# Optimization experiments

Measured on AMD Instinct MI355X. Metric: run time of the kernel, lower is better.

The kernel has to match this reference:

```python
import jax, jax.numpy as jnp
import numpy as np

D = 768      # embedding_dim
H = 12       # num_heads
HS = D // H  # head_size = 64
B, T, TC = 8, 1024, 256
FF = 4 * D
EPS = 1e-5


def _layernorm(x, w, b):
    mu = jnp.mean(x, axis=-1, keepdims=True)
    var = jnp.mean((x - mu) ** 2, axis=-1, keepdims=True)
    return (x - mu) / jnp.sqrt(var + EPS) * w + b


def _mha(x_q, x_kv, Wq, bq, Wk, bk, Wv, bv):
    # Batched equivalent of the per-head Python loop: weights stacked as [H, D, HS].
    q = jnp.einsum('btd,hde->bhte', x_q, Wq) + bq[None, :, None, :]
    k = jnp.einsum('bsd,hde->bhse', x_kv, Wk) + bk[None, :, None, :]
    v = jnp.einsum('bsd,hde->bhse', x_kv, Wv) + bv[None, :, None, :]
    scale = HS ** (-0.5)  # original scales by C**-0.5 with C = head_size
    wei = jax.nn.softmax(jnp.einsum('bhte,bhse->bhts', q, k) * scale, axis=-1)
    o = jnp.einsum('bhts,bhse->bhte', wei, v)  # [B,H,T,HS]
    # torch.cat over heads on dim=-1 == transpose then merge head dims
    return o.transpose(0, 2, 1, 3).reshape(o.shape[0], o.shape[2], H * HS)


def setup_inputs() -> dict:
    key = jax.random.key(0)
    ks = jax.random.split(key, 20)
    s = 0.02
    inp = {
        'img_embedding': jax.random.normal(ks[0], (B, T, D), jnp.float32),
        'context': jax.random.normal(ks[1], (B, TC, D), jnp.float32),
        'ln1_w': jnp.ones((D,), jnp.float32), 'ln1_b': jnp.zeros((D,), jnp.float32),
        'sWq': jax.random.normal(ks[2], (H, D, HS), jnp.float32) * s,
        'sbq': jnp.zeros((H, HS), jnp.float32),
        'sWk': jax.random.normal(ks[3], (H, D, HS), jnp.float32) * s,
        'sbk': jnp.zeros((H, HS), jnp.float32),
        'sWv': jax.random.normal(ks[4], (H, D, HS), jnp.float32) * s,
        'sbv': jnp.zeros((H, HS), jnp.float32),
        'ln2_w': jnp.ones((D,), jnp.float32), 'ln2_b': jnp.zeros((D,), jnp.float32),
        'cWq': jax.random.normal(ks[5], (H, D, HS), jnp.float32) * s,
        'cbq': jnp.zeros((H, HS), jnp.float32),
        'cWk': jax.random.normal(ks[6], (H, D, HS), jnp.float32) * s,
        'cbk': jnp.zeros((H, HS), jnp.float32),
        'cWv': jax.random.normal(ks[7], (H, D, HS), jnp.float32) * s,
        'cbv': jnp.zeros((H, HS), jnp.float32),
        'ln3_w': jnp.ones((D,), jnp.float32), 'ln3_b': jnp.zeros((D,), jnp.float32),
        'W1': jax.random.normal(ks[8], (D, FF), jnp.float32) * s,
        'b1': jnp.zeros((FF,), jnp.float32),
        'W2': jax.random.normal(ks[9], (FF, D), jnp.float32) * s,
        'b2': jnp.zeros((D,), jnp.float32),
    }
    return inp


def reference(img_embedding, context, ln1_w, ln1_b, sWq, sbq, sWk, sbk, sWv, sbv,
              ln2_w, ln2_b, cWq, cbq, cWk, cbk, cWv, cbv, ln3_w, ln3_b,
              W1, b1, W2, b2):
    x = img_embedding
    x = x + _mha(_layernorm(x, ln1_w, ln1_b), _layernorm(x, ln1_w, ln1_b),
                 sWq, sbq, sWk, sbk, sWv, sbv)
    x = x + _mha(_layernorm(x, ln2_w, ln2_b), context,
                 cWq, cbq, cWk, cbk, cWv, cbv)
    h = _layernorm(x, ln3_w, ln3_b)
    ff = jax.nn.silu(h @ W1 + b1) @ W2 + b2
    return x + ff
```

## Files before the change

kernel.cpp:

```cpp
#include <hip/hip_runtime.h>
#include <hip/hip_bf16.h>


#define D_EMB 768
#define N_HEADS 12
#define HEAD 64
#define B_SZ 8
#define T_IMG 1024
#define T_CTX 256
#define FF_DIM 3072
#define ROWS_IMG (B_SZ * T_IMG)
#define ROWS_CTX (B_SZ * T_CTX)
#define BIGCOL (1 << 28)
#define PART_STRIDE (ROWS_IMG * D_EMB)

typedef __bf16 bf16x8 __attribute__((ext_vector_type(8)));
typedef __bf16 bf16x4 __attribute__((ext_vector_type(4)));
typedef float f32x4 __attribute__((ext_vector_type(4)));

__device__ __forceinline__ void gld16(const void* g, void* l) {
    __builtin_amdgcn_global_load_lds(
        (const __attribute__((address_space(1))) unsigned int*)g,
        (__attribute__((address_space(3))) unsigned int*)l, 16, 0, 0);
}

__global__ __launch_bounds__(256) void cvt_bf16_kernel(const float* __restrict__ src,
                                                       __bf16* __restrict__ dst, int n4) {
    int i = blockIdx.x * 256 + threadIdx.x;
    if (i >= n4) return;
    float4 v = ((const float4*)src)[i];
    __bf16* d = dst + i * 4;
    d[0] = (__bf16)v.x; d[1] = (__bf16)v.y; d[2] = (__bf16)v.z; d[3] = (__bf16)v.w;
}

__global__ __launch_bounds__(256) void reduce_w2_kernel(
    const __bf16* __restrict__ P, const float* __restrict__ b2,
    float* __restrict__ X) {
    int i = blockIdx.x * 256 + threadIdx.x;
    int base = i * 4;
    int col = base % D_EMB;
    bf16x4 p0 = *(const bf16x4*)&P[base];
    bf16x4 p1 = *(const bf16x4*)&P[PART_STRIDE + base];
    float4 x = *(float4*)&X[base];
    float4 bb = *(const float4*)&b2[col];
    x.x += (float)p0[0] + (float)p1[0] + bb.x;
    x.y += (float)p0[1] + (float)p1[1] + bb.y;
    x.z += (float)p0[2] + (float)p1[2] + bb.z;
    x.w += (float)p0[3] + (float)p1[3] + bb.w;
    *(float4*)&X[base] = x;
}

__global__ __launch_bounds__(256) void transpose_cvt_kernel(
    const float* __restrict__ src, __bf16* __restrict__ dst,
    int src_rows, int src_cols) {
    __shared__ float tile[64][65];
    int tid = threadIdx.x;
    int r0 = blockIdx.y * 64, c0 = blockIdx.x * 64;
    int lr = tid >> 4, lc = (tid & 15) * 4;
#pragma unroll
    for (int i = 0; i < 4; i++) {
        float4 v = *(const float4*)&src[(size_t)(r0 + i * 16 + lr) * src_cols + c0 + lc];
        tile[i * 16 + lr][lc] = v.x; tile[i * 16 + lr][lc + 1] = v.y;
        tile[i * 16 + lr][lc + 2] = v.z; tile[i * 16 + lr][lc + 3] = v.w;
    }
    __syncthreads();
#pragma unroll
    for (int i = 0; i < 4; i++) {
        int cc = i * 16 + lr;
        int rr = (tid & 15) * 4;
        bf16x4 o;
#pragma unroll
        for (int j = 0; j < 4; j++) o[j] = (__bf16)tile[rr + j][cc];
        *(bf16x4*)&dst[(size_t)(c0 + cc) * src_rows + r0 + rr] = o;
    }
}

__global__ __launch_bounds__(256) void repack_qkv_t_kernel(
    const float* __restrict__ Wq, const float* __restrict__ Wk, const float* __restrict__ Wv,
    const float* __restrict__ bq, const float* __restrict__ bk, const float* __restrict__ bv,
    __bf16* __restrict__ Wt, float* __restrict__ bp) {
    __shared__ float tile[64][65];
    int tid = threadIdx.x;
    int which = blockIdx.y / 12, h = blockIdx.y - which * 12;
    int d0 = blockIdx.x * 64;
    const float* W = (which == 0) ? Wq : ((which == 1) ? Wk : Wv);
    const float* src = W + ((size_t)h * D_EMB + d0) * HEAD;
    int lr = tid >> 4, lc = (tid & 15) * 4;
#pragma unroll
    for (int i = 0; i < 4; i++) {
        float4 v = *(const float4*)&src[(size_t)(i * 16 + lr) * HEAD + lc];
        tile[i * 16 + lr][lc] = v.x; tile[i * 16 + lr][lc + 1] = v.y;
        tile[i * 16 + lr][lc + 2] = v.z; tile[i * 16 + lr][lc + 3] = v.w;
    }
    __syncthreads();
#pragma unroll
    for (int i = 0; i < 4; i++) {
        int e = i * 16 + lr;
        int dd = (tid & 15) * 4;
        bf16x4 o;
#pragma unroll
        for (int j = 0; j < 4; j++) o[j] = (__bf16)tile[dd + j][e];
        *(bf16x4*)&Wt[(size_t)(which * 768 + h * 64 + e) * D_EMB + d0 + dd] = o;
    }
    if (blockIdx.x == 0 && tid < 64) {
        const float* bb = (which == 0) ? bq : ((which == 1) ? bk : bv);
        bp[which * 768 + h * 64 + tid] = bb[h * 64 + tid];
    }
}

__global__ __launch_bounds__(256) void ln_kernel(const float* __restrict__ x,
                                                 const float* __restrict__ lw,
                                                 const float* __restrict__ lb,
                                                 __bf16* __restrict__ y) {
    int row = blockIdx.x;
    int tid = threadIdx.x;
    const float* xr = x + (size_t)row * D_EMB;
    float a0 = xr[tid], a1 = xr[tid + 256], a2 = xr[tid + 512];
    float s = a0 + a1 + a2;
    float ss = a0 * a0 + a1 * a1 + a2 * a2;
#pragma unroll
    for (int off = 32; off > 0; off >>= 1) {
        s += __shfl_down(s, off, 64);
        ss += __shfl_down(ss, off, 64);
    }
    __shared__ float red[8];
    __shared__ float stats[2];
    int wv = tid >> 6, lane = tid & 63;
    if (lane == 0) { red[wv] = s; red[4 + wv] = ss; }
    __syncthreads();
    if (tid == 0) {
        float S = red[0] + red[1] + red[2] + red[3];
        float SS = red[4] + red[5] + red[6] + red[7];
        float mu = S * (1.0f / D_EMB);
        float var = SS * (1.0f / D_EMB) - mu * mu;
        stats[0] = mu;
        stats[1] = rsqrtf(var + 1e-5f);
    }
    __syncthreads();
    float mu = stats[0], rs = stats[1];
    __bf16* yr = y + (size_t)row * D_EMB;
    yr[tid]       = (__bf16)((a0 - mu) * rs * lw[tid]       + lb[tid]);
    yr[tid + 256] = (__bf16)((a1 - mu) * rs * lw[tid + 256] + lb[tid + 256]);
    yr[tid + 512] = (__bf16)((a2 - mu) * rs * lw[tid + 512] + lb[tid + 512]);
}

__device__ __forceinline__ bf16x8 lds_frag(const __bf16* h, int row, int kk, int quad) {
    int off = (kk * 32 + quad * 8) ^ ((row & 7) << 3);
    return *(const bf16x8*)&h[row * 64 + off];
}

__global__ __launch_bounds__(256) void mfma_gemm_bt(
    const __bf16* __restrict__ A, int lda,
    const __bf16* __restrict__ Bt, int ldb,
    const float* __restrict__ bias,
    __bf16* __restrict__ Cb, int ldc,
    int Kc, int act, int qlimit,
    __bf16* __restrict__ VTout, int vtok, int vcol0, int kcol0, int kcol1,
    float* __restrict__ Xres) {
    __shared__ __bf16 As[128 * 64];
    __shared__ __bf16 Bs[128 * 64];
    int tid = threadIdx.x;
    int kz = blockIdx.z;
    int gx = gridDim.x;
    int nwg = gx * gridDim.y;
    int orig = blockIdx.y * gx + blockIdx.x;
    int swz = (orig & 7) * (nwg >> 3) + (orig >> 3);
    int bx = swz % gx, by = swz / gx;

    int w = tid >> 6, lane = tid & 63;
    int c = lane & 15, quad = lane >> 4;
    int wm = (w >> 1) * 64, wn = (w & 1) * 64;

    f32x4 acc[4][4];
#pragma unroll
    for (int i = 0; i < 4; i++)
#pragma unroll
        for (int j = 0; j < 4; j++) acc[i][j] = (f32x4){0.f, 0.f, 0.f, 0.f};

    int srow = tid >> 3;
    int scol = ((tid & 7) * 8) ^ ((srow & 7) * 8);
    const __bf16* Ag = A + (size_t)(by * 128 + srow) * lda + (size_t)kz * Kc + scol;
    const __bf16* Bg = Bt + (size_t)(bx * 128 + srow) * ldb + (size_t)kz * Kc + scol;
    char* AsB = (char*)As + w * 1024;
    char* BsB = (char*)Bs + w * 1024;

    for (int k0 = 0; k0 < Kc; k0 += 64) {
#pragma unroll
        for (int j = 0; j < 4; j++) {
            gld16(Ag + (size_t)(j * 32) * lda + k0, AsB + j * 4096);
            gld16(Bg + (size_t)(j * 32) * ldb + k0, BsB + j * 4096);
        }
        __syncthreads();
#pragma unroll
        for (int kk = 0; kk < 2; kk++) {
            bf16x8 af[4], bfr[4];
#pragma unroll
            for (int mi = 0; mi < 4; mi++)
                af[mi] = lds_frag(As, wm + mi * 16 + c, kk, quad);
#pragma unroll
            for (int ni = 0; ni < 4; ni++)
                bfr[ni] = lds_frag(Bs, wn + ni * 16 + c, kk, quad);
#pragma unroll
            for (int mi = 0; mi < 4; mi++)
#pragma unroll
                for (int ni = 0; ni < 4; ni++)
                    acc[mi][ni] = __builtin_amdgcn_mfma_f32_16x16x32_bf16(
                        bfr[ni], af[mi], acc[mi][ni], 0, 0, 0);
        }
        __syncthreads();
    }

#pragma unroll
    for (int mi = 0; mi < 4; mi++) {
#pragma unroll
        for (int ni = 0; ni < 4; ni++) {
            int row = by * 128 + wm + mi * 16 + c;
            int colbase = bx * 128 + wn + ni * 16 + quad * 4;
            float bvv[4] = {0.f, 0.f, 0.f, 0.f};
            if (bias && kz == 0) {
                float4 b4 = *(const float4*)&bias[colbase];
                bvv[0] = b4.x; bvv[1] = b4.y; bvv[2] = b4.z; bvv[3] = b4.w;
            }
            float qs = (colbase < qlimit) ? 0.125f : 1.0f;
            float v[4];
#pragma unroll
            for (int r = 0; r < 4; r++) {
                float t = (acc[mi][ni][r] + bvv[r]) * qs;
                if (act == 1) t = t / (1.0f + __expf(-t));
                v[r] = t;
            }
            if (Xres) {
                float4 x4 = *(float4*)&Xres[(size_t)row * D_EMB + colbase];
                x4.x += v[0]; x4.y += v[1]; x4.z += v[2]; x4.w += v[3];
                *(float4*)&Xres[(size_t)row * D_EMB + colbase] = x4;
            } else if (VTout && colbase >= vcol0) {
                int hc = colbase - vcol0;
                int hh = hc >> 6, ebase = hc & 63;
                int tok = row;
#pragma unroll
                for (int r = 0; r < 4; r++) {
                    int e = ebase + r;
                    int sl = ((((tok >> 3) & 7) ^ (e & 7)) << 3) | (tok & 7);
                    VTout[(size_t)(hh * 64 + e) * vtok + (tok & ~63) + sl] = (__bf16)v[r];
                }
            } else if (colbase >= kcol0 && colbase < kcol1) {
                int hc = colbase - kcol0;
                int hh = hc >> 6, ebase = hc & 63;
                int tok = row;
                int es = (((ebase >> 3) ^ (tok & 7)) << 3) | (ebase & 7);
                bf16x4 pv;
#pragma unroll
                for (int r = 0; r < 4; r++) pv[r] = (__bf16)v[r];
                *(bf16x4*)&Cb[(size_t)tok * ldc + kcol0 + hh * 64 + es] = pv;
            } else {
                __bf16* dst = Cb + (size_t)kz * PART_STRIDE;
                bf16x4 pv;
#pragma unroll
                for (int r = 0; r < 4; r++) pv[r] = (__bf16)v[r];
                *(bf16x4*)&dst[(size_t)row * ldc + colbase] = pv;
            }
        }
    }
}

__global__ __launch_bounds__(128, 2) void mfma_attn(
    const __bf16* __restrict__ Q, int qld,
    const __bf16* __restrict__ Kp, int kld,
    const __bf16* __restrict__ VTg, int vtok,
    int kv_tokens, float* __restrict__ X, const float* __restrict__ Xin) {
    __shared__ __bf16 Kt[64 * 64];
    __shared__ __bf16 VT[80 * 64];
    __shared__ __bf16 Ps[128 * 76];
    int tid = threadIdx.x;
    int bh = blockIdx.x % 96;
    int qt = blockIdx.x / 96;
    int b = bh / N_HEADS, h = bh - b * N_HEADS;
    int w = tid >> 6, lane = tid & 63, c = lane & 15, quad = lane >> 4;
    int q0 = qt * 128;

    for (int i = tid; i < 16 * 64; i += 128)
        VT[64 * 64 + i] = (i < 64) ? (__bf16)1.0f : (__bf16)0.0f;

    {
        const __bf16* Qg = Q + (size_t)(b * T_IMG + q0 + (tid >> 3)) * qld
                           + h * HEAD + (tid & 7) * 8;
        char* QsB = (char*)Ps + w * 1024;
#pragma unroll
        for (int j = 0; j < 8; j++)
            gld16(Qg + (size_t)j * 16 * qld, QsB + j * 2048);
    }
    __syncthreads();
    bf16x8 qa[4][2];
#pragma unroll
    for (int st = 0; st < 4; st++)
#pragma unroll
        for (int ch = 0; ch < 2; ch++)
            qa[st][ch] = *(const bf16x8*)&Ps[(w * 64 + st * 16 + c) * 64 + ch * 32 + quad * 8];
    __syncthreads();

    f32x4 o[4][5];
#pragma unroll
    for (int st = 0; st < 4; st++)
#pragma unroll
        for (int ut = 0; ut < 5; ut++) o[st][ut] = (f32x4){0.f, 0.f, 0.f, 0.f};

    char* KtB = (char*)Kt + w * 1024;
    char* VtB = (char*)VT + w * 1024;
    int ntiles = kv_tokens >> 6;
    for (int t = 0; t < ntiles; t++) {
        const __bf16* Kg = Kp + (size_t)(b * kv_tokens + t * 64 + (tid >> 3)) * kld
                           + h * HEAD + (tid & 7) * 8;
        const __bf16* Vg = VTg + (size_t)(h * HEAD + (tid >> 3)) * vtok
                           + b * kv_tokens + t * 64 + (tid & 7) * 8;
#pragma unroll
        for (int j = 0; j < 4; j++) {
            gld16(Kg + (size_t)j * 16 * kld, KtB + j * 2048);
            gld16(Vg + (size_t)j * 16 * vtok, VtB + j * 2048);
        }
        __syncthreads();

        bf16x8 kb[4][2];
#pragma unroll
        for (int nt = 0; nt < 4; nt++)
#pragma unroll
            for (int ch = 0; ch < 2; ch++)
                kb[nt][ch] = *(const bf16x8*)&Kt[(nt * 16 + c) * 64
                                + (((ch * 4 + quad) ^ (c & 7)) << 3)];
#pragma unroll
        for (int st = 0; st < 4; st++) {
            f32x4 s[4];
#pragma unroll
            for (int nt = 0; nt < 4; nt++) {
                s[nt] = (f32x4){0.f, 0.f, 0.f, 0.f};
                s[nt] = __builtin_amdgcn_mfma_f32_16x16x32_bf16(kb[nt][0], qa[st][0], s[nt], 0, 0, 0);
                s[nt] = __builtin_amdgcn_mfma_f32_16x16x32_bf16(kb[nt][1], qa[st][1], s[nt], 0, 0, 0);
            }
#pragma unroll
            for (int nt = 0; nt < 4; nt++) {
                bf16x4 pk;
#pragma unroll
                for (int r = 0; r < 4; r++) pk[r] = (__bf16)__expf(s[nt][r]);
                *(bf16x4*)&Ps[(size_t)(w * 64 + st * 16 + c) * 76 + nt * 16 + quad * 4] = pk;
            }
        }
        __syncthreads();

        bf16x8 vb[5][2];
#pragma unroll
        for (int ut = 0; ut < 5; ut++)
#pragma unroll
            for (int ch = 0; ch < 2; ch++)
                vb[ut][ch] = *(const bf16x8*)&VT[(ut * 16 + c) * 64
                                + (((ch * 4 + quad) ^ (c & 7)) << 3)];
#pragma unroll
        for (int st = 0; st < 4; st++) {
            bf16x8 pa0 = *(const bf16x8*)&Ps[(w * 64 + st * 16 + c) * 76 + quad * 8];
            bf16x8 pa1 = *(const bf16x8*)&Ps[(w * 64 + st * 16 + c) * 76 + 32 + quad * 8];
#pragma unroll
            for (int ut = 0; ut < 5; ut++) {
                o[st][ut] = __builtin_amdgcn_mfma_f32_16x16x32_bf16(pa0, vb[ut][0], o[st][ut], 0, 0, 0);
                o[st][ut] = __builtin_amdgcn_mfma_f32_16x16x32_bf16(pa1, vb[ut][1], o[st][ut], 0, 0, 0);
            }
        }
        __syncthreads();
    }

#pragma unroll
    for (int st = 0; st < 4; st++) {
        float lr[4];
#pragma unroll
        for (int r = 0; r < 4; r++) lr[r] = __shfl(o[st][4][r], lane & 48, 64);
#pragma unroll
        for (int ut = 0; ut < 4; ut++) {
#pragma unroll
            for (int r = 0; r < 4; r++) {
                int row = b * T_IMG + q0 + w * 64 + st * 16 + quad * 4 + r;
                int col = h * HEAD + ut * 16 + c;
                size_t idx = (size_t)row * D_EMB + col;
                float base = Xin ? Xin[idx] : X[idx];
                X[idx] = base + o[st][ut][r] / lr[r];
            }
        }
    }
}

extern "C" void kernel_launch(void* const* d_in, const int* in_sizes, int n_in,
                              void* d_out, int out_size, void* d_ws, size_t ws_size,
                              hipStream_t stream) {
    const float* img  = (const float*)d_in[0];
    const float* ctx  = (const float*)d_in[1];
    const float* ln1w = (const float*)d_in[2];  const float* ln1b = (const float*)d_in[3];
    const float* sWq  = (const float*)d_in[4];  const float* sbq  = (const float*)d_in[5];
    const float* sWk  = (const float*)d_in[6];  const float* sbk  = (const float*)d_in[7];
    const float* sWv  = (const float*)d_in[8];  const float* sbv  = (const float*)d_in[9];
    const float* ln2w = (const float*)d_in[10]; const float* ln2b = (const float*)d_in[11];
    const float* cWq  = (const float*)d_in[12]; const float* cbq  = (const float*)d_in[13];
    const float* cWk  = (const float*)d_in[14]; const float* cbk  = (const float*)d_in[15];
    const float* cWv  = (const float*)d_in[16]; const float* cbv  = (const float*)d_in[17];
    const float* ln3w = (const float*)d_in[18]; const float* ln3b = (const float*)d_in[19];
    const float* W1   = (const float*)d_in[20]; const float* b1   = (const float*)d_in[21];
    const float* W2   = (const float*)d_in[22]; const float* b2   = (const float*)d_in[23];

    float* X = (float*)d_out;

    char* p = (char*)d_ws;
    __bf16* LNb  = (__bf16*)p; p += (size_t)ROWS_IMG * D_EMB * 2;
    __bf16* VTg  = (__bf16*)p; p += (size_t)12 * 64 * ROWS_IMG * 2;
    __bf16* BIG  = (__bf16*)p; p += (size_t)ROWS_IMG * FF_DIM * 2;
    __bf16* ctxb = (__bf16*)p; p += (size_t)ROWS_CTX * D_EMB * 2;
    __bf16* Wt   = (__bf16*)p; p += (size_t)2304 * 768 * 2;
    __bf16* cWt  = (__bf16*)p; p += (size_t)2304 * 768 * 2;
    __bf16* W1t  = (__bf16*)p; p += (size_t)FF_DIM * 768 * 2;
    __bf16* W2t  = (__bf16*)p; p += (size_t)768 * FF_DIM * 2;
    __bf16* VTc  = (__bf16*)p; p += (size_t)12 * 64 * ROWS_CTX * 2;
    float*  bp   = (float*)p;  p += 2304 * 4;
    float*  cbp  = (float*)p;  p += 2304 * 4;
    __bf16* Pk   = LNb;
    __bf16* QKVb = BIG;
    __bf16* Qc   = BIG;
    __bf16* KVc  = BIG + (size_t)ROWS_IMG * 768;
    __bf16* FFh  = BIG;

    cvt_bf16_kernel<<<(ROWS_CTX * D_EMB / 4 + 255) / 256, 256, 0, stream>>>(
        ctx, ctxb, ROWS_CTX * D_EMB / 4);
    repack_qkv_t_kernel<<<dim3(12, 36), 256, 0, stream>>>(
        sWq, sWk, sWv, sbq, sbk, sbv, Wt, bp);
    repack_qkv_t_kernel<<<dim3(12, 36), 256, 0, stream>>>(
        cWq, cWk, cWv, cbq, cbk, cbv, cWt, cbp);
    transpose_cvt_kernel<<<dim3(FF_DIM / 64, 768 / 64), 256, 0, stream>>>(
        W1, W1t, 768, FF_DIM);
    transpose_cvt_kernel<<<dim3(768 / 64, FF_DIM / 64), 256, 0, stream>>>(
        W2, W2t, FF_DIM, 768);

    ln_kernel<<<ROWS_IMG, 256, 0, stream>>>(img, ln1w, ln1b, LNb);
    mfma_gemm_bt<<<dim3(2304 / 128, ROWS_IMG / 128), 256, 0, stream>>>(
        LNb, D_EMB, Wt, D_EMB, bp, QKVb, 2304, D_EMB, 0, 768,
        VTg, ROWS_IMG, 1536, 768, 1536, nullptr);
    mfma_attn<<<96 * 8, 128, 0, stream>>>(
        QKVb, 2304, QKVb + 768, 2304, VTg, ROWS_IMG, T_IMG, X, img);

    ln_kernel<<<ROWS_IMG, 256, 0, stream>>>(X, ln2w, ln2b, LNb);
    mfma_gemm_bt<<<dim3(768 / 128, ROWS_IMG / 128), 256, 0, stream>>>(
        LNb, D_EMB, cWt, D_EMB, cbp, Qc, 768, D_EMB, 0, 768,
        nullptr, 0, BIGCOL, BIGCOL, BIGCOL, nullptr);
    mfma_gemm_bt<<<dim3(1536 / 128, ROWS_CTX / 128), 256, 0, stream>>>(
        ctxb, D_EMB, cWt + (size_t)768 * 768, D_EMB, cbp + 768,
        KVc, 1536, D_EMB, 0, 0,
        VTc, ROWS_CTX, 768, 0, 768, nullptr);
    mfma_attn<<<96 * 8, 128, 0, stream>>>(
        Qc, 768, KVc, 1536, VTc, ROWS_CTX, T_CTX, X, nullptr);

    ln_kernel<<<ROWS_IMG, 256, 0, stream>>>(X, ln3w, ln3b, LNb);
    mfma_gemm_bt<<<dim3(FF_DIM / 128, ROWS_IMG / 128), 256, 0, stream>>>(
        LNb, D_EMB, W1t, D_EMB, b1, FFh, FF_DIM, D_EMB, 1, 0,
        nullptr, 0, BIGCOL, BIGCOL, BIGCOL, nullptr);
    mfma_gemm_bt<<<dim3(768 / 128, ROWS_IMG / 128, 2), 256, 0, stream>>>(
        FFh, FF_DIM, W2t, FF_DIM, nullptr, Pk, D_EMB, 1536, 0, 0,
        nullptr, 0, BIGCOL, BIGCOL, BIGCOL, nullptr);
    reduce_w2_kernel<<<ROWS_IMG * D_EMB / 4 / 256, 256, 0, stream>>>(Pk, b2, X);
}
```

Measured before the change: 463.7 us.

## Double-buffer GEMM K-tiles in LDS to overlap global loads with MFMA

Replaces the single-buffered 64-wide K-step GEMM loop with a double-buffered 32-wide K-step pipeline. The next tile is fetched via global_load_lds into the alternate buffer while MFMAs run on the current one, and the LDS layout and XOR swizzle are changed to a 32-column row format. The goal is to hide global memory latency behind compute. In exchange the K step is halved, so there are twice as many barriers per K, and the loop assumes Kc/32 is handled correctly when odd.

```diff
diff --git a/kernel.cpp b/kernel.cpp
--- a/kernel.cpp
+++ b/kernel.cpp
@@ -144,9 +144,9 @@
     yr[tid + 512] = (__bf16)((a2 - mu) * rs * lw[tid + 512] + lb[tid + 512]);
 }
 
-__device__ __forceinline__ bf16x8 lds_frag(const __bf16* h, int row, int kk, int quad) {
-    int off = (kk * 32 + quad * 8) ^ ((row & 7) << 3);
-    return *(const bf16x8*)&h[row * 64 + off];
+__device__ __forceinline__ bf16x8 lds_frag32(const __bf16* buf, int row, int quad) {
+    int off = (quad ^ ((row >> 1) & 3)) * 8;
+    return *(const bf16x8*)&buf[row * 32 + off];
 }
 
 __global__ __launch_bounds__(256) void mfma_gemm_bt(
@@ -157,8 +157,7 @@
     int Kc, int act, int qlimit,
     __bf16* __restrict__ VTout, int vtok, int vcol0, int kcol0, int kcol1,
     float* __restrict__ Xres) {
-    __shared__ __bf16 As[128 * 64];
-    __shared__ __bf16 Bs[128 * 64];
+    __shared__ __bf16 SM[4 * 4096];
     int tid = threadIdx.x;
     int kz = blockIdx.z;
     int gx = gridDim.x;
@@ -177,38 +176,59 @@
 #pragma unroll
         for (int j = 0; j < 4; j++) acc[i][j] = (f32x4){0.f, 0.f, 0.f, 0.f};
 
-    int srow = tid >> 3;
-    int scol = ((tid & 7) * 8) ^ ((srow & 7) * 8);
+    int srow = tid >> 2;
+    int scol = ((tid & 3) ^ ((srow >> 1) & 3)) * 8;
     const __bf16* Ag = A + (size_t)(by * 128 + srow) * lda + (size_t)kz * Kc + scol;
     const __bf16* Bg = Bt + (size_t)(bx * 128 + srow) * ldb + (size_t)kz * Kc + scol;
-    char* AsB = (char*)As + w * 1024;
-    char* BsB = (char*)Bs + w * 1024;
-
-    for (int k0 = 0; k0 < Kc; k0 += 64) {
-#pragma unroll
-        for (int j = 0; j < 4; j++) {
-            gld16(Ag + (size_t)(j * 32) * lda + k0, AsB + j * 4096);
-            gld16(Bg + (size_t)(j * 32) * ldb + k0, BsB + j * 4096);
-        }
+    char* SB = (char*)SM;
+    char* A0 = SB + w * 1024;
+    char* B0 = SB + 8192 + w * 1024;
+    char* A1 = SB + 16384 + w * 1024;
+    char* B1 = SB + 24576 + w * 1024;
+
+#define STAGE32(kcol, dA, dB)                                   \
+    do {                                                        \
+        gld16(Ag + (kcol), dA);                                 \
+        gld16(Ag + (size_t)64 * lda + (kcol), dA + 4096);       \
+        gld16(Bg + (kcol), dB);                                 \
+        gld16(Bg + (size_t)64 * ldb + (kcol), dB + 4096);       \
+    } while (0)
+
+#define COMPUTE32(Ab, Bb)                                                     \
+    do {                                                                      \
+        bf16x8 af[4], bfr[4];                                                 \
+        _Pragma("unroll")                                                     \
+        for (int mi = 0; mi < 4; mi++)                                        \
+            af[mi] = lds_frag32((Ab), wm + mi * 16 + c, quad);                \
+        _Pragma("unroll")                                                     \
+        for (int ni = 0; ni < 4; ni++)                                        \
+            bfr[ni] = lds_frag32((Bb), wn + ni * 16 + c, quad);               \
+        _Pragma("unroll")                                                     \
+        for (int mi = 0; mi < 4; mi++)                                        \
+            _Pragma("unroll")                                                 \
+            for (int ni = 0; ni < 4; ni++)                                    \
+                acc[mi][ni] = __builtin_amdgcn_mfma_f32_16x16x32_bf16(        \
+                    bfr[ni], af[mi], acc[mi][ni], 0, 0, 0);                   \
+    } while (0)
+
+    const __bf16* As0 = SM;
+    const __bf16* Bs0 = SM + 4096;
+    const __bf16* As1 = SM + 8192;
+    const __bf16* Bs1 = SM + 12288;
+
+    int nt = Kc >> 5;
+    STAGE32(0, A0, B0);
+    __syncthreads();
+    for (int t = 0; t < nt; t += 2) {
+        if (t + 1 < nt) STAGE32((t + 1) * 32, A1, B1);
+        COMPUTE32(As0, Bs0);
         __syncthreads();
-#pragma unroll
-        for (int kk = 0; kk < 2; kk++) {
-            bf16x8 af[4], bfr[4];
-#pragma unroll
-            for (int mi = 0; mi < 4; mi++)
-                af[mi] = lds_frag(As, wm + mi * 16 + c, kk, quad);
-#pragma unroll
-            for (int ni = 0; ni < 4; ni++)
-                bfr[ni] = lds_frag(Bs, wn + ni * 16 + c, kk, quad);
-#pragma unroll
-            for (int mi = 0; mi < 4; mi++)
-#pragma unroll
-                for (int ni = 0; ni < 4; ni++)
-                    acc[mi][ni] = __builtin_amdgcn_mfma_f32_16x16x32_bf16(
-                        bfr[ni], af[mi], acc[mi][ni], 0, 0, 0);
-        }
+        if (t + 2 < nt) STAGE32((t + 2) * 32, A0, B0);
+        COMPUTE32(As1, Bs1);
         __syncthreads();
     }
+#undef STAGE32
+#undef COMPUTE32
 
 #pragma unroll
     for (int mi = 0; mi < 4; mi++) {
```

Result: slower. 481.4 us (+3.8%).
